# Optimization experiments

Measured on AMD Instinct MI355X. Metric: run time of the kernel, lower is better.

The kernel has to match this reference:

```python
import jax, jax.numpy as jnp
import numpy as np

B, C, Hsp, Wsp = 16, 256, 64, 64
NUM_HEADS = 8
NORM_GROUPS = 4
EPS = 1e-5


def setup_inputs() -> dict:
    key = jax.random.key(0)
    ks = jax.random.split(key, 6)
    x = jax.random.normal(ks[0], (B, C, Hsp, Wsp), dtype=jnp.float32)
    gn_weight = jnp.ones((C,), dtype=jnp.float32)
    gn_bias = jnp.zeros((C,), dtype=jnp.float32)
    # Conv2d 1x1 kernels == dense matrices over channels
    qkv_weight = jax.random.normal(ks[1], (3 * C, C), dtype=jnp.float32) * (1.0 / np.sqrt(C))
    proj_weight = jax.random.normal(ks[2], (C, C), dtype=jnp.float32) * (1.0 / np.sqrt(C))
    proj_bias = jax.random.normal(ks[3], (C,), dtype=jnp.float32) * 0.01
    return {
        "x": x,
        "gn_weight": gn_weight,
        "gn_bias": gn_bias,
        "qkv_weight": qkv_weight,
        "proj_weight": proj_weight,
        "proj_bias": proj_bias,
    }


def reference(x, gn_weight, gn_bias, qkv_weight, proj_weight, proj_bias):
    b, c, h, w = x.shape
    hd = c // NUM_HEADS  # head dim
    n = h * w            # number of spatial tokens

    # GroupNorm over (c//G, h, w) per group, then per-channel affine
    xg = x.reshape(b, NORM_GROUPS, -1)
    mu = jnp.mean(xg, axis=-1, keepdims=True)
    var = jnp.mean(jnp.square(xg - mu), axis=-1, keepdims=True)
    xn = ((xg - mu) * jax.lax.rsqrt(var + EPS)).reshape(b, c, h, w)
    xn = xn * gn_weight[None, :, None, None] + gn_bias[None, :, None, None]

    # 1x1 conv (no bias) == channel matmul; output channel order matches torch view(b,3,H,d,h,w)
    qkv = jnp.einsum('bchw,oc->bohw', xn, qkv_weight)  # [b, 3c, h, w]
    qkv = qkv.reshape(b, 3, NUM_HEADS, hd, n)
    q, k, v = qkv[:, 0], qkv[:, 1], qkv[:, 2]          # each [b, H, d, n]

    # Linear (kernelized) attention: softmax over keys' token axis
    k = jax.nn.softmax(k, axis=-1)
    att = jnp.einsum('bhdn,bhen->bhde', k, v)          # [b, H, d, d]
    out = jnp.einsum('bhde,bhdn->bhen', att, q)        # [b, H, d, n]
    out = out.reshape(b, c, h, w)

    # Output 1x1 conv with bias
    return jnp.einsum('bchw,oc->bohw', out, proj_weight) + proj_bias[None, :, None, None]
```

## Files before the change

kernel.cpp:

```cpp
#include <hip/hip_runtime.h>
#include <hip/hip_bf16.h>


typedef __attribute__((ext_vector_type(4))) float f32x4;
typedef __attribute__((ext_vector_type(8))) short bf16x8;
typedef __attribute__((ext_vector_type(4))) short s16x4;
typedef __attribute__((ext_vector_type(8))) unsigned short u16x8;

__device__ inline float b2f(unsigned short u) {
  unsigned int x = ((unsigned int)u) << 16;
  float f; __builtin_memcpy(&f, &x, 4); return f;
}
__device__ inline unsigned short f2b(float f) {
  unsigned int x; __builtin_memcpy(&x, &f, 4);
  x += 0x7FFFu + ((x >> 16) & 1u);
  return (unsigned short)(x >> 16);
}

__global__ void __launch_bounds__(256) k_gn_partial(const float* __restrict__ x,
                                                    float* __restrict__ partials) {
  int blk = blockIdx.x;
  int grp = blk >> 4;
  int part = blk & 15;
  const float* base = x + (size_t)grp * 262144 + (size_t)part * 16384;
  int t = threadIdx.x;
  float s = 0.f, s2 = 0.f;
  for (int i = 0; i < 16; ++i) {
    f32x4 v = *(const f32x4*)(base + (size_t)(i * 256 + t) * 4);
    s  += v[0] + v[1] + v[2] + v[3];
    s2 += v[0]*v[0] + v[1]*v[1] + v[2]*v[2] + v[3]*v[3];
  }
  for (int o = 32; o > 0; o >>= 1) { s += __shfl_down(s, o); s2 += __shfl_down(s2, o); }
  __shared__ float ls[4], ls2[4];
  int w = t >> 6;
  if ((t & 63) == 0) { ls[w] = s; ls2[w] = s2; }
  __syncthreads();
  if (t == 0) {
    partials[blk * 2] = ls[0] + ls[1] + ls[2] + ls[3];
    partials[blk * 2 + 1] = ls2[0] + ls2[1] + ls2[2] + ls2[3];
  }
}

__global__ void __launch_bounds__(256) k_finalize(const float* __restrict__ partials,
                                                  float* __restrict__ stats,
                                                  const float* __restrict__ qkvw,
                                                  unsigned short* __restrict__ Wb,
                                                  unsigned short* __restrict__ WqT) {
  int bx = blockIdx.x, t = threadIdx.x;
  if (bx == 0) {
    if (t < 64) {
      float S = 0.f, S2 = 0.f;
      for (int i = 0; i < 16; ++i) { S += partials[(t * 16 + i) * 2]; S2 += partials[(t * 16 + i) * 2 + 1]; }
      float mu = S * (1.f / 262144.f);
      float var = S2 * (1.f / 262144.f) - mu * mu;
      stats[t * 2] = mu;
      stats[t * 2 + 1] = rsqrtf(var + 1e-5f);
    }
  } else if (bx <= 192) {
    int idx = (bx - 1) * 256 + t;
    f32x4 v = *(const f32x4*)(qkvw + (size_t)idx * 4);
    s16x4 o;
    for (int i = 0; i < 4; ++i) o[i] = (short)f2b(v[i]);
    *(s16x4*)(Wb + (size_t)idx * 4) = o;
  } else {
    int bb = bx - 193;
    int c = bb * 16 + (t & 15);
    int d0 = (t >> 4) * 16;
    for (int i = 0; i < 16; ++i) {
      int d = d0 + i;
      WqT[(size_t)c * 256 + d] = f2b(qkvw[(size_t)d * 256 + c]);
    }
  }
}

__global__ void __launch_bounds__(256) k_norm_t(const float* __restrict__ x,
                                                const float* __restrict__ stats,
                                                const float* __restrict__ gamma,
                                                const float* __restrict__ beta,
                                                unsigned short* __restrict__ xnT) {
  int blk = blockIdx.x;
  int b = blk >> 8;
  int tile = blk & 255;
  int ct = tile >> 6;
  int nt = tile & 63;
  int c0 = ct * 64, n0 = nt * 64;
  __shared__ float T[64][65];
  int t = threadIdx.x;
  float mu = stats[(b * 4 + ct) * 2];
  float rs = stats[(b * 4 + ct) * 2 + 1];
  int cl = t >> 2, q4 = t & 3;
  float sc = gamma[c0 + cl] * rs;
  float off = beta[c0 + cl] - mu * sc;
  const float* xr = x + ((size_t)b * 256 + c0 + cl) * 4096 + n0;
  for (int p = 0; p < 4; ++p) {
    int col = p * 16 + q4 * 4;
    f32x4 v = *(const f32x4*)(xr + col);
    for (int i = 0; i < 4; ++i) T[cl][col + i] = v[i] * sc + off;
  }
  __syncthreads();
  int nl = t >> 2, cc = t & 3;
  u16x8 o0, o1;
  for (int i = 0; i < 8; ++i) o0[i] = f2b(T[cc * 16 + i][nl]);
  for (int i = 0; i < 8; ++i) o1[i] = f2b(T[cc * 16 + 8 + i][nl]);
  unsigned short* dst = xnT + ((size_t)b * 4096 + n0 + nl) * 256 + c0 + cc * 16;
  *(u16x8*)dst = o0;
  *(u16x8*)(dst + 8) = o1;
}

template<bool OUT_BF16, bool ADD_BIAS>
__global__ void __launch_bounds__(256)
k_gemm_bt(const unsigned short* __restrict__ A,
          const unsigned short* __restrict__ B,
          void* __restrict__ Cv,
          const float* __restrict__ bias,
          long sA, long sB, long sC, int ldc) {
  __shared__ unsigned short LA[128][32];
  __shared__ unsigned short LB[128][32];
  const int t = threadIdx.x;
  const unsigned short* Ab = A + (size_t)blockIdx.z * sA + (size_t)blockIdx.x * 128 * 256;
  const unsigned short* Bb = B + (size_t)blockIdx.z * sB + (size_t)blockIdx.y * 128 * 256;
  const int wave = t >> 6, lane = t & 63;
  const int wm = wave >> 1, wn = wave & 1;
  const int g = lane >> 4, r = lane & 15;
  const int rA = t >> 2, sslot = t & 3;
  const int ws0 = 8 * (sslot ^ (rA & 3));
  const int rslot = 8 * (g ^ (r & 3));
  const unsigned short* ag = Ab + (size_t)rA * 256 + 8 * sslot;
  const unsigned short* bg = Bb + (size_t)rA * 256 + 8 * sslot;
  u16x8 pa0 = *(const u16x8*)(ag);
  u16x8 pa1 = *(const u16x8*)(ag + 64 * 256);
  u16x8 pb0 = *(const u16x8*)(bg);
  u16x8 pb1 = *(const u16x8*)(bg + 64 * 256);
  f32x4 acc[4][4] = {};
  for (int kt = 0; kt < 8; ++kt) {
    if (kt) __syncthreads();
    *(u16x8*)&LA[rA][ws0] = pa0;  *(u16x8*)&LA[rA + 64][ws0] = pa1;
    *(u16x8*)&LB[rA][ws0] = pb0;  *(u16x8*)&LB[rA + 64][ws0] = pb1;
    __syncthreads();
    if (kt < 7) {
      int off = (kt + 1) * 32;
      pa0 = *(const u16x8*)(ag + off);  pa1 = *(const u16x8*)(ag + 64 * 256 + off);
      pb0 = *(const u16x8*)(bg + off);  pb1 = *(const u16x8*)(bg + 64 * 256 + off);
    }
    bf16x8 af[4], bfr[4];
    for (int i = 0; i < 4; ++i) {
      af[i]  = *(const bf16x8*)&LA[wm * 64 + i * 16 + r][rslot];
      bfr[i] = *(const bf16x8*)&LB[wn * 64 + i * 16 + r][rslot];
    }
    for (int mi = 0; mi < 4; ++mi)
      for (int ni = 0; ni < 4; ++ni)
        acc[mi][ni] = __builtin_amdgcn_mfma_f32_16x16x32_bf16(af[mi], bfr[ni], acc[mi][ni], 0, 0, 0);
  }
  const int m0 = blockIdx.x * 128 + wm * 64;
  const int n0 = blockIdx.y * 128 + wn * 64;
  if (OUT_BF16) {
    unsigned short* C = (unsigned short*)Cv + (size_t)blockIdx.z * sC;
    for (int mi = 0; mi < 4; ++mi)
      for (int ni = 0; ni < 4; ++ni) {
        int row = m0 + mi * 16 + 4 * g;
        int col = n0 + ni * 16 + r;
        for (int reg = 0; reg < 4; ++reg)
          C[(size_t)(row + reg) * ldc + col] = f2b(acc[mi][ni][reg]);
      }
  } else {
    float* C = (float*)Cv + (size_t)blockIdx.z * sC;
    for (int mi = 0; mi < 4; ++mi)
      for (int ni = 0; ni < 4; ++ni) {
        int row = m0 + mi * 16 + 4 * g;
        int col = n0 + ni * 16 + r;
        for (int reg = 0; reg < 4; ++reg) {
          float v = acc[mi][ni][reg];
          if (ADD_BIAS) v += bias[row + reg];
          C[(size_t)(row + reg) * ldc + col] = v;
        }
      }
  }
}

__global__ void __launch_bounds__(256) k_att(const unsigned short* __restrict__ kv,
                                             float* __restrict__ attg,
                                             float* __restrict__ rsums) {
  int ns = blockIdx.x, h = blockIdx.y, b = blockIdx.z;
  int hb = b * 8 + h;
  const unsigned short* kbase = kv + ((size_t)b * 512 + h * 32) * 4096 + ns * 1024;
  const unsigned short* vbase = kbase + (size_t)256 * 4096;
  __shared__ unsigned short P[32][136];
  __shared__ unsigned short V[32][136];
  __shared__ float psum[32][8];
  __shared__ float attbuf[4][32][33];
  int t = threadIdx.x;
  int d = t >> 3, j = t & 7;
  int wave = t >> 6, lane = t & 63, g = lane >> 4, r = lane & 15;
  float rsum = 0.f;
  f32x4 acc[2][2] = {};
  for (int c = 0; c < 8; ++c) {
    int n0 = c * 128;
    const unsigned short* ksrc = kbase + (size_t)d * 4096 + n0 + j * 16;
    const unsigned short* vsrc = vbase + (size_t)d * 4096 + n0 + j * 16;
    u16x8 ka = *(const u16x8*)ksrc;
    u16x8 kb2 = *(const u16x8*)(ksrc + 8);
    u16x8 va = *(const u16x8*)vsrc;
    u16x8 vb2 = *(const u16x8*)(vsrc + 8);
    u16x8 p0, p1;
    for (int i = 0; i < 8; ++i) { float e = __expf(b2f(ka[i]));  rsum += e; p0[i] = f2b(e); }
    for (int i = 0; i < 8; ++i) { float e = __expf(b2f(kb2[i])); rsum += e; p1[i] = f2b(e); }
    if (c) __syncthreads();
    *(u16x8*)&P[d][j * 16] = p0;     *(u16x8*)&P[d][j * 16 + 8] = p1;
    *(u16x8*)&V[d][j * 16] = va;     *(u16x8*)&V[d][j * 16 + 8] = vb2;
    __syncthreads();
    bf16x8 pf[2], vf[2];
    for (int i = 0; i < 2; ++i) {
      pf[i] = *(const bf16x8*)&P[i * 16 + r][wave * 32 + 8 * g];
      vf[i] = *(const bf16x8*)&V[i * 16 + r][wave * 32 + 8 * g];
    }
    for (int mi = 0; mi < 2; ++mi)
      for (int ni = 0; ni < 2; ++ni)
        acc[mi][ni] = __builtin_amdgcn_mfma_f32_16x16x32_bf16(pf[mi], vf[ni], acc[mi][ni], 0, 0, 0);
  }
  __syncthreads();
  psum[d][j] = rsum;
  for (int mi = 0; mi < 2; ++mi)
    for (int ni = 0; ni < 2; ++ni)
      for (int reg = 0; reg < 4; ++reg)
        attbuf[wave][mi * 16 + 4 * g + reg][ni * 16 + r] = acc[mi][ni][reg];
  __syncthreads();
  if (t < 32) {
    float s = 0.f;
    for (int i = 0; i < 8; ++i) s += psum[t][i];
    atomicAdd(&rsums[hb * 32 + t], s);
  }
  float* dst = attg + (size_t)hb * 1024;
  for (int i = 0; i < 4; ++i) {
    int idx = t * 4 + i;
    int dd = idx >> 5, ee = idx & 31;
    atomicAdd(&dst[idx],
              attbuf[0][dd][ee] + attbuf[1][dd][ee] + attbuf[2][dd][ee] + attbuf[3][dd][ee]);
  }
}

__global__ void __launch_bounds__(256) k_makeM(const float* __restrict__ attg,
                                               const float* __restrict__ rsums,
                                               const float* __restrict__ projw,
                                               unsigned short* __restrict__ Mb) {
  int blk = blockIdx.x;
  int b = blk >> 3, h = blk & 7;
  __shared__ float attL[32][33];
  __shared__ float invs[32];
  int t = threadIdx.x;
  if (t < 32) invs[t] = 1.f / rsums[blk * 32 + t];
  const float* asrc = attg + (size_t)blk * 1024;
  {
    f32x4 v = *(const f32x4*)(asrc + (size_t)t * 4);
    int idx = t * 4;
    for (int i = 0; i < 4; ++i) attL[(idx + i) >> 5][(idx + i) & 31] = v[i];
  }
  __syncthreads();
  float pw[32];
  const float* ps = projw + (size_t)t * 256 + h * 32;
  for (int i = 0; i < 8; ++i) {
    f32x4 v = *(const f32x4*)(ps + i * 4);
    pw[i * 4 + 0] = v[0]; pw[i * 4 + 1] = v[1]; pw[i * 4 + 2] = v[2]; pw[i * 4 + 3] = v[3];
  }
  unsigned short* dst = Mb + ((size_t)b * 256 + t) * 256 + h * 32;
  for (int dd = 0; dd < 32; ++dd) {
    float s = 0.f;
    for (int e = 0; e < 32; ++e) s += pw[e] * attL[dd][e];
    dst[dd] = f2b(s * invs[dd]);
  }
}

extern "C" void kernel_launch(void* const* d_in, const int* in_sizes, int n_in,
                              void* d_out, int out_size, void* d_ws, size_t ws_size,
                              hipStream_t stream) {
  (void)in_sizes; (void)n_in; (void)out_size; (void)ws_size;
  const float* x     = (const float*)d_in[0];
  const float* gn_w  = (const float*)d_in[1];
  const float* gn_b  = (const float*)d_in[2];
  const float* qkvw  = (const float*)d_in[3];
  const float* projw = (const float*)d_in[4];
  const float* projb = (const float*)d_in[5];

  char* ws = (char*)d_ws;
  float*          partials = (float*)(ws);
  float*          stats    = (float*)(ws + 8192);
  unsigned short* Wb       = (unsigned short*)(ws + 16384);
  unsigned short* Mb       = (unsigned short*)(ws + 409600);
  float*          attg     = (float*)(ws + 2506752);
  float*          rsums    = (float*)(ws + 3031040);
  unsigned short* WqT      = (unsigned short*)(ws + 3047424);
  unsigned short* M2       = (unsigned short*)(ws + 3178496);
  unsigned short* xnT      = (unsigned short*)(ws + 8388608);
  unsigned short* kvb      = (unsigned short*)(ws + 8388608 + 33554432);

  k_gn_partial<<<1024, 256, 0, stream>>>(x, partials);
  k_finalize<<<209, 256, 0, stream>>>(partials, stats, qkvw, Wb, WqT);
  k_norm_t<<<4096, 256, 0, stream>>>(x, stats, gn_w, gn_b, xnT);
  k_gemm_bt<true, false><<<dim3(4, 32, 16), 256, 0, stream>>>(
      Wb + 65536, xnT, (void*)kvb, nullptr, 0L, 1048576L, 2097152L, 4096);
  hipMemsetAsync(attg, 0, 540672, stream);
  k_att<<<dim3(4, 8, 16), 256, 0, stream>>>(kvb, attg, rsums);
  k_makeM<<<128, 256, 0, stream>>>(attg, rsums, projw, Mb);
  k_gemm_bt<true, false><<<dim3(2, 2, 16), 256, 0, stream>>>(
      Mb, WqT, (void*)M2, nullptr, 65536L, 0L, 65536L, 256);
  k_gemm_bt<false, true><<<dim3(2, 32, 16), 256, 0, stream>>>(
      M2, xnT, d_out, projb, 65536L, 1048576L, 1048576L, 4096);
}
```

Before: 241.5 us.

## Fuse K/V projection GEMM into attention kernel and add dedicated final GEMM

The K/V projection is now computed inside the attention kernel. Each block holds its head's K and V weight rows in registers, multiplies them against xnT tiles with MFMA, applies exp and row sums, and accumulates the d×d context through LDS. This removes the 32 MB bf16 KV intermediate write and re-read and one launch. The final output GEMM is replaced by a specialised kernel with a 256×64 tile that reads A directly from global, double-buffers B in swizzled LDS and prefetches the next slice. The trade-off is more register pressure and a serialised per-chunk sync in the fused kernel.

New measurement: 249.9 us. 1.03x slower.

```diff
diff --git a/kernel.cpp b/kernel.cpp
--- a/kernel.cpp
+++ b/kernel.cpp
@@ -105,6 +105,96 @@
   unsigned short* dst = xnT + ((size_t)b * 4096 + n0 + nl) * 256 + c0 + cc * 16;
   *(u16x8*)dst = o0;
   *(u16x8*)(dst + 8) = o1;
+}
+
+__global__ void __launch_bounds__(256) k_attfused(const unsigned short* __restrict__ Wb,
+                                                  const unsigned short* __restrict__ xnT,
+                                                  float* __restrict__ attg,
+                                                  float* __restrict__ rsums) {
+  const int bx = blockIdx.x;
+  const int b = bx >> 2, ns = bx & 3, h = blockIdx.y;
+  const int hb = b * 8 + h;
+  const int t = threadIdx.x;
+  const int wave = t >> 6, lane = t & 63;
+  const int g = lane >> 4, r = lane & 15;
+  const int rh = wave >> 1;
+  const int ch = wave & 1;
+  __shared__ unsigned short PL[2][32][72];
+  __shared__ unsigned short VL[2][32][72];
+
+  const unsigned short* Wrow = Wb + (size_t)(256 + rh * 256 + h * 32) * 256;
+  bf16x8 af[2][8];
+#pragma unroll
+  for (int rt = 0; rt < 2; ++rt)
+#pragma unroll
+    for (int kt = 0; kt < 8; ++kt)
+      af[rt][kt] = *(const bf16x8*)(Wrow + (size_t)(rt * 16 + r) * 256 + kt * 32 + 8 * g);
+
+  const unsigned short* Xb = xnT + ((size_t)b * 4096 + ns * 1024 + ch * 32 + r) * 256 + 8 * g;
+  f32x4 attacc = {0.f, 0.f, 0.f, 0.f};
+  float rs[2][4] = {{0.f,0.f,0.f,0.f},{0.f,0.f,0.f,0.f}};
+
+  for (int c = 0; c < 16; ++c) {
+    const int cur = c & 1;
+    const unsigned short* Xc = Xb + (size_t)(c * 64) * 256;
+    bf16x8 bfr[8][2];
+#pragma unroll
+    for (int kt = 0; kt < 8; ++kt)
+#pragma unroll
+      for (int ct = 0; ct < 2; ++ct)
+        bfr[kt][ct] = *(const bf16x8*)(Xc + (size_t)(ct * 16) * 256 + kt * 32);
+    f32x4 sacc[2][2] = {};
+#pragma unroll
+    for (int kt = 0; kt < 8; ++kt)
+#pragma unroll
+      for (int rt = 0; rt < 2; ++rt)
+#pragma unroll
+        for (int ct = 0; ct < 2; ++ct)
+          sacc[rt][ct] = __builtin_amdgcn_mfma_f32_16x16x32_bf16(
+              af[rt][kt], bfr[kt][ct], sacc[rt][ct], 0, 0, 0);
+    if (rh == 0) {
+#pragma unroll
+      for (int rt = 0; rt < 2; ++rt)
+#pragma unroll
+        for (int ct = 0; ct < 2; ++ct)
+#pragma unroll
+          for (int reg = 0; reg < 4; ++reg) {
+            float e = __expf(sacc[rt][ct][reg]);
+            rs[rt][reg] += e;
+            PL[cur][rt * 16 + 4 * g + reg][ch * 32 + ct * 16 + r] = f2b(e);
+          }
+    } else {
+#pragma unroll
+      for (int rt = 0; rt < 2; ++rt)
+#pragma unroll
+        for (int ct = 0; ct < 2; ++ct)
+#pragma unroll
+          for (int reg = 0; reg < 4; ++reg)
+            VL[cur][rt * 16 + 4 * g + reg][ch * 32 + ct * 16 + r] = f2b(sacc[rt][ct][reg]);
+    }
+    __syncthreads();
+#pragma unroll
+    for (int ks = 0; ks < 2; ++ks) {
+      bf16x8 pa = *(const bf16x8*)&PL[cur][rh * 16 + r][ks * 32 + 8 * g];
+      bf16x8 vb = *(const bf16x8*)&VL[cur][ch * 16 + r][ks * 32 + 8 * g];
+      attacc = __builtin_amdgcn_mfma_f32_16x16x32_bf16(pa, vb, attacc, 0, 0, 0);
+    }
+  }
+  float* ab = attg + (size_t)hb * 1024;
+#pragma unroll
+  for (int reg = 0; reg < 4; ++reg)
+    atomicAdd(&ab[(rh * 16 + 4 * g + reg) * 32 + ch * 16 + r], attacc[reg]);
+  if (rh == 0) {
+#pragma unroll
+    for (int rt = 0; rt < 2; ++rt)
+#pragma unroll
+      for (int reg = 0; reg < 4; ++reg) {
+        float v = rs[rt][reg];
+        v += __shfl_xor(v, 1); v += __shfl_xor(v, 2);
+        v += __shfl_xor(v, 4); v += __shfl_xor(v, 8);
+        if (r == 0) atomicAdd(&rsums[hb * 32 + rt * 16 + 4 * g + reg], v);
+      }
+  }
 }
 
 template<bool OUT_BF16, bool ADD_BIAS>
@@ -177,67 +267,6 @@
   }
 }
 
-__global__ void __launch_bounds__(256) k_att(const unsigned short* __restrict__ kv,
-                                             float* __restrict__ attg,
-                                             float* __restrict__ rsums) {
-  int ns = blockIdx.x, h = blockIdx.y, b = blockIdx.z;
-  int hb = b * 8 + h;
-  const unsigned short* kbase = kv + ((size_t)b * 512 + h * 32) * 4096 + ns * 1024;
-  const unsigned short* vbase = kbase + (size_t)256 * 4096;
-  __shared__ unsigned short P[32][136];
-  __shared__ unsigned short V[32][136];
-  __shared__ float psum[32][8];
-  __shared__ float attbuf[4][32][33];
-  int t = threadIdx.x;
-  int d = t >> 3, j = t & 7;
-  int wave = t >> 6, lane = t & 63, g = lane >> 4, r = lane & 15;
-  float rsum = 0.f;
-  f32x4 acc[2][2] = {};
-  for (int c = 0; c < 8; ++c) {
-    int n0 = c * 128;
-    const unsigned short* ksrc = kbase + (size_t)d * 4096 + n0 + j * 16;
-    const unsigned short* vsrc = vbase + (size_t)d * 4096 + n0 + j * 16;
-    u16x8 ka = *(const u16x8*)ksrc;
-    u16x8 kb2 = *(const u16x8*)(ksrc + 8);
-    u16x8 va = *(const u16x8*)vsrc;
-    u16x8 vb2 = *(const u16x8*)(vsrc + 8);
-    u16x8 p0, p1;
-    for (int i = 0; i < 8; ++i) { float e = __expf(b2f(ka[i]));  rsum += e; p0[i] = f2b(e); }
-    for (int i = 0; i < 8; ++i) { float e = __expf(b2f(kb2[i])); rsum += e; p1[i] = f2b(e); }
-    if (c) __syncthreads();
-    *(u16x8*)&P[d][j * 16] = p0;     *(u16x8*)&P[d][j * 16 + 8] = p1;
-    *(u16x8*)&V[d][j * 16] = va;     *(u16x8*)&V[d][j * 16 + 8] = vb2;
-    __syncthreads();
-    bf16x8 pf[2], vf[2];
-    for (int i = 0; i < 2; ++i) {
-      pf[i] = *(const bf16x8*)&P[i * 16 + r][wave * 32 + 8 * g];
-      vf[i] = *(const bf16x8*)&V[i * 16 + r][wave * 32 + 8 * g];
-    }
-    for (int mi = 0; mi < 2; ++mi)
-      for (int ni = 0; ni < 2; ++ni)
-        acc[mi][ni] = __builtin_amdgcn_mfma_f32_16x16x32_bf16(pf[mi], vf[ni], acc[mi][ni], 0, 0, 0);
-  }
-  __syncthreads();
-  psum[d][j] = rsum;
-  for (int mi = 0; mi < 2; ++mi)
-    for (int ni = 0; ni < 2; ++ni)
-      for (int reg = 0; reg < 4; ++reg)
-        attbuf[wave][mi * 16 + 4 * g + reg][ni * 16 + r] = acc[mi][ni][reg];
-  __syncthreads();
-  if (t < 32) {
-    float s = 0.f;
-    for (int i = 0; i < 8; ++i) s += psum[t][i];
-    atomicAdd(&rsums[hb * 32 + t], s);
-  }
-  float* dst = attg + (size_t)hb * 1024;
-  for (int i = 0; i < 4; ++i) {
-    int idx = t * 4 + i;
-    int dd = idx >> 5, ee = idx & 31;
-    atomicAdd(&dst[idx],
-              attbuf[0][dd][ee] + attbuf[1][dd][ee] + attbuf[2][dd][ee] + attbuf[3][dd][ee]);
-  }
-}
-
 __global__ void __launch_bounds__(256) k_makeM(const float* __restrict__ attg,
                                                const float* __restrict__ rsums,
                                                const float* __restrict__ projw,
@@ -269,6 +298,53 @@
   }
 }
 
+__global__ void __launch_bounds__(256) k_gemm_final(const unsigned short* __restrict__ M2,
+                                                    const unsigned short* __restrict__ xnT,
+                                                    float* __restrict__ out,
+                                                    const float* __restrict__ bias) {
+  const int nt = blockIdx.x, b = blockIdx.y;
+  const unsigned short* Ab = M2 + (size_t)b * 65536;
+  const unsigned short* Bb = xnT + ((size_t)b * 4096 + nt * 64) * 256;
+  float* Cb = out + (size_t)b * 1048576 + (size_t)nt * 64;
+  __shared__ unsigned short LB[2][64][32];
+  const int t = threadIdx.x;
+  const int wave = t >> 6, lane = t & 63, g = lane >> 4, r = lane & 15;
+  const int srow = t >> 2, sslot = t & 3;
+  const int ws0 = 8 * (sslot ^ (srow & 3));
+  const int rslot = 8 * (g ^ (r & 3));
+  const unsigned short* bg = Bb + (size_t)srow * 256 + 8 * sslot;
+  const unsigned short* ar = Ab + (size_t)(wave * 64 + r) * 256 + 8 * g;
+  u16x8 pb = *(const u16x8*)bg;
+  f32x4 acc[4][4] = {};
+  for (int kt = 0; kt < 8; ++kt) {
+    const int cur = kt & 1;
+    *(u16x8*)&LB[cur][srow][ws0] = pb;
+    __syncthreads();
+    if (kt < 7) pb = *(const u16x8*)(bg + (kt + 1) * 32);
+    bf16x8 af[4], bfr[4];
+#pragma unroll
+    for (int mi = 0; mi < 4; ++mi)
+      af[mi] = *(const bf16x8*)(ar + (size_t)(mi * 16) * 256 + kt * 32);
+#pragma unroll
+    for (int ni = 0; ni < 4; ++ni)
+      bfr[ni] = *(const bf16x8*)&LB[cur][ni * 16 + r][rslot];
+#pragma unroll
+    for (int mi = 0; mi < 4; ++mi)
+#pragma unroll
+      for (int ni = 0; ni < 4; ++ni)
+        acc[mi][ni] = __builtin_amdgcn_mfma_f32_16x16x32_bf16(af[mi], bfr[ni], acc[mi][ni], 0, 0, 0);
+  }
+#pragma unroll
+  for (int mi = 0; mi < 4; ++mi) {
+    const int row = wave * 64 + mi * 16 + 4 * g;
+#pragma unroll
+    for (int ni = 0; ni < 4; ++ni)
+#pragma unroll
+      for (int reg = 0; reg < 4; ++reg)
+        Cb[(size_t)(row + reg) * 4096 + ni * 16 + r] = acc[mi][ni][reg] + bias[row + reg];
+  }
+}
+
 extern "C" void kernel_launch(void* const* d_in, const int* in_sizes, int n_in,
                               void* d_out, int out_size, void* d_ws, size_t ws_size,
                               hipStream_t stream) {
@@ -290,18 +366,14 @@
   unsigned short* WqT      = (unsigned short*)(ws + 3047424);
   unsigned short* M2       = (unsigned short*)(ws + 3178496);
   unsigned short* xnT      = (unsigned short*)(ws + 8388608);
-  unsigned short* kvb      = (unsigned short*)(ws + 8388608 + 33554432);
 
   k_gn_partial<<<1024, 256, 0, stream>>>(x, partials);
   k_finalize<<<209, 256, 0, stream>>>(partials, stats, qkvw, Wb, WqT);
   k_norm_t<<<4096, 256, 0, stream>>>(x, stats, gn_w, gn_b, xnT);
-  k_gemm_bt<true, false><<<dim3(4, 32, 16), 256, 0, stream>>>(
-      Wb + 65536, xnT, (void*)kvb, nullptr, 0L, 1048576L, 2097152L, 4096);
-  hipMemsetAsync(attg, 0, 540672, stream);
-  k_att<<<dim3(4, 8, 16), 256, 0, stream>>>(kvb, attg, rsums);
+  (void)hipMemsetAsync(attg, 0, 540672, stream);
+  k_attfused<<<dim3(64, 8), 256, 0, stream>>>(Wb, xnT, attg, rsums);
   k_makeM<<<128, 256, 0, stream>>>(attg, rsums, projw, Mb);
   k_gemm_bt<true, false><<<dim3(2, 2, 16), 256, 0, stream>>>(
       Mb, WqT, (void*)M2, nullptr, 65536L, 0L, 65536L, 256);
-  k_gemm_bt<false, true><<<dim3(2, 32, 16), 256, 0, stream>>>(
-      M2, xnT, d_out, projb, 65536L, 1048576L, 1048576L, 4096);
-}
+  k_gemm_final<<<dim3(64, 16), 256, 0, stream>>>(M2, xnT, (float*)d_out, projb);
+}
```
